# Kernel optimization log

Hardware: AMD Instinct MI355X
Metric: run time of the kernel (lower is better)

Reference implementation:

```python
import jax, jax.numpy as jnp
import numpy as np

EPS = 1e-5

def _ln(x, g, b):
    mu = jnp.mean(x, -1, keepdims=True)
    var = jnp.mean(jnp.square(x - mu), -1, keepdims=True)
    return (x - mu) * jax.lax.rsqrt(var + EPS) * g + b

def _switch_moe(h, gw, gb, W1, b1, W2, b2):
    # h: [B,T,D]; top-1 switch routing over E experts
    probs = jax.nn.softmax(h @ gw + gb, axis=-1)        # [B,T,E]
    idx = jnp.argmax(probs, axis=-1)                    # [B,T]
    p = jnp.max(probs, axis=-1)[..., None]              # [B,T,1] top-1 gate prob
    out = jnp.zeros_like(h)
    E = W1.shape[0]
    for e in range(E):  # small fixed expert count
        y = jax.nn.gelu(h @ W1[e] + b1[e]) @ W2[e] + b2[e]
        out = out + jnp.where((idx == e)[..., None], p * y, 0.0)
    return out

def setup_inputs() -> dict:
    key = jax.random.key(0)
    B, T, D, F, E, TE, NB = 64, 196, 512, 2048, 8, 512, 2
    ks = jax.random.split(key, 16)
    s = 0.02
    return {
        "x": jax.random.normal(ks[0], (B, T, D), jnp.float32),
        "emb": jax.random.normal(ks[1], (B, TE), jnp.float32),
        "ln_g": jnp.ones((NB, D), jnp.float32),
        "ln_b": jnp.zeros((NB, D), jnp.float32),
        "gate_w": jax.random.normal(ks[2], (NB, D, E), jnp.float32) * s,
        "gate_b": jnp.zeros((NB, E), jnp.float32),
        "w1": jax.random.normal(ks[3], (NB, E, D, F), jnp.float32) * s,
        "b1": jnp.zeros((NB, E, F), jnp.float32),
        "w2": jax.random.normal(ks[4], (NB, E, F, D), jnp.float32) * s,
        "b2": jnp.zeros((NB, E, D), jnp.float32),
        "emb_w": jax.random.normal(ks[5], (TE, 2 * D), jnp.float32) * s,
        "emb_b": jnp.zeros((2 * D,), jnp.float32),
        "sn_g": jnp.ones((D,), jnp.float32),
        "sn_b": jnp.zeros((D,), jnp.float32),
        "out_w": jax.random.normal(ks[6], (D, D), jnp.float32) * s,
        "out_b": jnp.zeros((D,), jnp.float32),
    }

def reference(x, emb, ln_g, ln_b, gate_w, gate_b, w1, b1, w2, b2,
              emb_w, emb_b, sn_g, sn_b, out_w, out_b):
    NB = ln_g.shape[0]
    out = jnp.zeros_like(x)
    for br in range(NB):  # fixed small branch count; dropout = identity (eval)
        h = _ln(x, ln_g[br], ln_b[br])
        out = out + _switch_moe(h, gate_w[br], gate_b[br], w1[br], b1[br], w2[br], b2[br])
    out = out / NB
    # StylizationBlock (FiLM): norm, scale/shift from time emb, SiLU+Linear, residual
    eo = jax.nn.silu(emb) @ emb_w + emb_b            # [B,2D]
    scale, shift = jnp.split(eo[:, None, :], 2, axis=-1)  # [B,1,D] each
    h = _ln(out, sn_g, sn_b) * (1.0 + scale) + shift
    h = jax.nn.silu(h) @ out_w + out_b
    return x + h
```

## Files before the change

### kernel.cpp

```cpp
#include <hip/hip_runtime.h>
#include <hip/hip_bf16.h>

typedef unsigned short u16;
typedef unsigned int u32;

typedef short bf16v8 __attribute__((ext_vector_type(8)));
typedef float f32v4 __attribute__((ext_vector_type(4)));

constexpr int BB   = 64;
constexpr int TT   = 196;
constexpr int NTOK = BB * TT;
constexpr int DD   = 512;
constexpr int FF   = 2048;
constexpr int EE   = 8;
constexpr int NBR  = 2;
constexpr int GE   = NBR * EE;
constexpr int MT128 = 212;

__device__ __forceinline__ u16 f2bf(float f) {
    union { float f; u32 u; } v; v.f = f;
    u32 r = v.u + 0x7fffu + ((v.u >> 16) & 1u);
    return (u16)(r >> 16);
}

__device__ __forceinline__ float bf2f(u32 u) {
    union { u32 u; float f; } v; v.u = u << 16; return v.f;
}

__device__ __forceinline__ float wave_sum(float v) {
    #pragma unroll
    for (int m = 32; m > 0; m >>= 1) v += __shfl_xor(v, m, 64);
    return v;
}

__device__ __forceinline__ float gelu_tanh(float v) {
    float y = 1.595769122f * v + 0.071354816f * (v * v * v);
    return v / (1.0f + __expf(-y));
}

__device__ __forceinline__ float silu(float v) {
    return v / (1.0f + __expf(-v));
}

__device__ __forceinline__ void gload16(const u16* g, u16* l) {
    typedef const __attribute__((address_space(1))) unsigned gv_t;
    typedef __attribute__((address_space(3))) unsigned lv_t;
    __builtin_amdgcn_global_load_lds((gv_t*)g, (lv_t*)l, 16, 0, 0);
}

__device__ __forceinline__ void bar() {
    asm volatile("" ::: "memory");
    __builtin_amdgcn_s_barrier();
    asm volatile("" ::: "memory");
}

#define ASM_VMCNT4 asm volatile("s_waitcnt vmcnt(4)" ::: "memory")
#define ASM_VMCNT0 asm volatile("s_waitcnt vmcnt(0)" ::: "memory")
#define ASM_LGKM0  asm volatile("s_waitcnt lgkmcnt(0)" ::: "memory")

__global__ __launch_bounds__(256) void mtrans_eo_kernel(
    const float* __restrict__ w1, u16* __restrict__ w1t,
    const float* __restrict__ w2, u16* __restrict__ w2t,
    const float* __restrict__ ow, u16* __restrict__ owt,
    const float* __restrict__ emb, const float* __restrict__ emb_w,
    const float* __restrict__ emb_b, float* __restrict__ eo,
    int* __restrict__ cnt)
{
    __shared__ float tile[64][69];
    __shared__ float se[4][DD];
    int id = blockIdx.x;
    int t = threadIdx.x;

    if (id >= 8256) {
        int id2 = id - 8256;
        int cg = id2 & 3, bg = id2 >> 2;
        int b0 = bg * 4;
        int c0 = cg * 256 + t;
        for (int i = t; i < 4 * DD; i += 256) {
            int b = i >> 9, d = i & (DD - 1);
            se[b][d] = silu(emb[(size_t)(b0 + b) * DD + d]);
        }
        __syncthreads();
        float acc[4] = {0, 0, 0, 0};
        for (int k = 0; k < DD; ++k) {
            float wv = emb_w[(size_t)k * 1024 + c0];
            #pragma unroll
            for (int b = 0; b < 4; ++b) acc[b] += se[b][k] * wv;
        }
        float bb = emb_b[c0];
        #pragma unroll
        for (int b = 0; b < 4; ++b)
            eo[(size_t)(b0 + b) * 1024 + c0] = acc[b] + bb;
        return;
    }

    if (id == 0 && t < 16) cnt[t] = 0;

    const float* src; u16* dst; int R, C, rt, ct;
    if (id < 4096) {
        int e = id >> 8, rem = id & 255;
        R = DD; C = FF; rt = rem >> 5; ct = rem & 31;
        src = w1 + (size_t)e * R * C; dst = w1t + (size_t)e * R * C;
    } else if (id < 8192) {
        int e = (id - 4096) >> 8, rem = (id - 4096) & 255;
        R = FF; C = DD; rt = rem >> 3; ct = rem & 7;
        src = w2 + (size_t)e * R * C; dst = w2t + (size_t)e * R * C;
    } else {
        int rem = id - 8192;
        R = DD; C = DD; rt = rem >> 3; ct = rem & 7;
        src = ow; dst = owt;
    }
    int tx = t & 15, ty = t >> 4;
    int r0 = rt * 64, c0 = ct * 64;
    #pragma unroll
    for (int j = 0; j < 4; ++j) {
        int row = ty + j * 16;
        float4 v = *(const float4*)&src[(size_t)(r0 + row) * C + c0 + tx * 4];
        tile[row][tx * 4 + 0] = v.x;
        tile[row][tx * 4 + 1] = v.y;
        tile[row][tx * 4 + 2] = v.z;
        tile[row][tx * 4 + 3] = v.w;
    }
    __syncthreads();
    int wc = t & 7, wr0 = t >> 3;
    #pragma unroll
    for (int p = 0; p < 2; ++p) {
        int cc = wr0 + p * 32;
        u16 pk[8];
        #pragma unroll
        for (int i = 0; i < 8; ++i)
            pk[i] = f2bf(tile[wc * 8 + i][cc]);
        uint4 v;
        v.x = (u32)pk[0] | ((u32)pk[1] << 16);
        v.y = (u32)pk[2] | ((u32)pk[3] << 16);
        v.z = (u32)pk[4] | ((u32)pk[5] << 16);
        v.w = (u32)pk[6] | ((u32)pk[7] << 16);
        *(uint4*)&dst[(size_t)(c0 + cc) * R + r0 + wc * 8] = v;
    }
}

__global__ __launch_bounds__(256) void ln_gate_kernel(
    const float* __restrict__ x, const float* __restrict__ ln_g, const float* __restrict__ ln_b,
    const float* __restrict__ gate_w, const float* __restrict__ gate_b,
    u16* __restrict__ hA, u16* __restrict__ hB,
    int* __restrict__ idxb, float* __restrict__ pbuf)
{
    int wave = threadIdx.x >> 6, lane = threadIdx.x & 63;
    int tok = blockIdx.x * 4 + wave;
    const float* xr = x + (size_t)tok * DD + lane * 8;
    float4 v0 = *(const float4*)xr;
    float4 v1 = *(const float4*)(xr + 4);
    float xs[8] = {v0.x, v0.y, v0.z, v0.w, v1.x, v1.y, v1.z, v1.w};
    float s = 0.f, ss = 0.f;
    #pragma unroll
    for (int i = 0; i < 8; ++i) { s += xs[i]; ss += xs[i] * xs[i]; }
    s = wave_sum(s); ss = wave_sum(ss);
    float mu = s * (1.0f / DD);
    float var = ss * (1.0f / DD) - mu * mu;
    float rstd = rsqrtf(var + 1e-5f);

    #pragma unroll
    for (int br = 0; br < NBR; ++br) {
        u16* hb = br ? hB : hA;
        float part[8] = {0, 0, 0, 0, 0, 0, 0, 0};
        u16 hu[8];
        #pragma unroll
        for (int i = 0; i < 8; ++i) {
            int d = lane * 8 + i;
            float g = ln_g[br * DD + d], b = ln_b[br * DD + d];
            float h = (xs[i] - mu) * rstd * g + b;
            hu[i] = f2bf(h);
            const float* gw = gate_w + ((size_t)br * DD + d) * EE;
            float4 g0 = *(const float4*)gw;
            float4 g1 = *(const float4*)(gw + 4);
            part[0] += h * g0.x; part[1] += h * g0.y; part[2] += h * g0.z; part[3] += h * g0.w;
            part[4] += h * g1.x; part[5] += h * g1.y; part[6] += h * g1.z; part[7] += h * g1.w;
        }
        uint4 pk;
        pk.x = (u32)hu[0] | ((u32)hu[1] << 16);
        pk.y = (u32)hu[2] | ((u32)hu[3] << 16);
        pk.z = (u32)hu[4] | ((u32)hu[5] << 16);
        pk.w = (u32)hu[6] | ((u32)hu[7] << 16);
        *(uint4*)(hb + (size_t)tok * DD + lane * 8) = pk;

        float logit[8];
        #pragma unroll
        for (int e = 0; e < 8; ++e)
            logit[e] = wave_sum(part[e]) + gate_b[br * EE + e];
        float m = logit[0]; int bi = 0;
        #pragma unroll
        for (int e = 1; e < 8; ++e)
            if (logit[e] > m) { m = logit[e]; bi = e; }
        float sum = 0.f;
        #pragma unroll
        for (int e = 0; e < 8; ++e) sum += __expf(logit[e] - m);
        if (lane == 0) {
            idxb[br * NTOK + tok] = bi;
            pbuf[br * NTOK + tok] = 1.0f / sum;
        }
    }
}

__global__ __launch_bounds__(256) void route_kernel(
    const int* __restrict__ idxb, int* __restrict__ cnt, int* __restrict__ list)
{
    __shared__ int lcnt[GE];
    __shared__ int gbase[GE];
    int tid = threadIdx.x;
    int t = blockIdx.x * 256 + tid;
    if (tid < GE) lcnt[tid] = 0;
    __syncthreads();
    int e0 = idxb[t];
    int e1 = EE + idxb[NTOK + t];
    int r0 = atomicAdd(&lcnt[e0], 1);
    int r1 = atomicAdd(&lcnt[e1], 1);
    __syncthreads();
    if (tid < GE) {
        int c = lcnt[tid];
        gbase[tid] = c ? atomicAdd(&cnt[tid], c) : 0;
    }
    __syncthreads();
    list[(size_t)e0 * NTOK + gbase[e0] + r0] = t;
    list[(size_t)e1 * NTOK + gbase[e1] + r1] = t;
}

__global__ void tilestart_kernel(const int* __restrict__ cnt, int* __restrict__ meta)
{
    int lane = threadIdx.x;
    if (lane < 16) {
        int pbv = 0;
        for (int k = 0; k < lane; ++k) pbv += cnt[k];
        meta[lane] = pbv;
    }
    if (lane == 16) {
        int n = 0;
        for (int k = 0; k < 16; ++k) n += (cnt[k] + 127) >> 7;
        meta[33] = n;
    }
    for (int j = lane; j < MT128; j += 64) {
        int ge = -1, start = 0, tt = 0;
        #pragma unroll
        for (int k = 0; k < 16; ++k) {
            int mt = (cnt[k] + 127) >> 7;
            if (ge < 0) {
                if (j < start + mt) { ge = k; tt = j - start; }
                else start += mt;
            }
        }
        if (ge >= 0) meta[64 + j] = (ge << 20) | tt;
    }
}

template<int MODE>
__global__ __launch_bounds__(256, 3) void gemm_tile(
    const u16* __restrict__ A0, const u16* __restrict__ A1,
    const u16* __restrict__ Bt,
    const int* __restrict__ meta, const int* __restrict__ cnt,
    const int* __restrict__ list, const float* __restrict__ pbuf,
    const float* __restrict__ bias,
    u16* __restrict__ uout, u16* __restrict__ moeout,
    const float* __restrict__ xres, float* __restrict__ dout)
{
    constexpr int K = (MODE == 1) ? FF : DD;
    constexpr int N = (MODE == 0) ? FF : DD;
    constexpr int NSTEP = K / 32;

    __shared__ __align__(16) u16 As[2][128 * 32];
    __shared__ __align__(16) u16 Bs[2][128 * 32];
    __shared__ int rowtok[128];
    __shared__ float rowp[128];

    int ntile = blockIdx.x;
    int ge = 0, rb = 0, cnt_e = 1 << 30, pb = 0;
    if constexpr (MODE != 2) {
        int j = blockIdx.y;
        if (j >= meta[33]) return;
        int ev = meta[64 + j];
        ge = ev >> 20;
        rb = (ev & 0xfffff) << 7;
        cnt_e = cnt[ge];
        pb = meta[ge];
    } else {
        rb = blockIdx.y * 128;
    }

    int tid = threadIdx.x, wave = tid >> 6, lane = tid & 63;
    int wm = wave >> 1, wn = wave & 1;
    int fr = lane & 15, fq = lane >> 4;
    int r0 = wave * 16 + (lane >> 2);
    int sc = (lane & 3) ^ ((lane >> 3) & 3);

    const u16* Abase;
    if constexpr (MODE == 0) Abase = (ge >= 8) ? A1 : A0;
    else                     Abase = A0;
    const u16* Bte = Bt + ((MODE == 2) ? (size_t)0 : (size_t)ge * FF * DD);

    const u16 *aSrc0, *aSrc1, *bSrc0, *bSrc1;
    if constexpr (MODE == 0) {
        int lb = ge * NTOK;
        int g0 = rb + r0, g1 = g0 + 64;
        int t0 = (g0 < cnt_e) ? list[lb + g0] : list[lb];
        int t1 = (g1 < cnt_e) ? list[lb + g1] : list[lb];
        aSrc0 = Abase + (size_t)t0 * K + sc * 8;
        aSrc1 = Abase + (size_t)t1 * K + sc * 8;
    } else {
        size_t base = (MODE == 1) ? (size_t)(pb + rb) : (size_t)rb;
        aSrc0 = Abase + (base + r0) * (size_t)K + sc * 8;
        aSrc1 = Abase + (base + r0 + 64) * (size_t)K + sc * 8;
    }
    {
        int nrow = ntile * 128 + r0;
        bSrc0 = Bte + (size_t)nrow * K + sc * 8;
        bSrc1 = Bte + (size_t)(nrow + 64) * K + sc * 8;
    }

    if constexpr (MODE == 1) {
        if (tid < 128) {
            int g = rb + tid;
            int tk = (g < cnt_e) ? list[ge * NTOK + g] : -1;
            rowtok[tid] = tk;
            rowp[tid] = (tk >= 0) ? pbuf[(ge >> 3) * NTOK + tk] : 0.f;
        }
        ASM_LGKM0;
    }

    f32v4 acc[4][4];
    #pragma unroll
    for (int mi = 0; mi < 4; ++mi)
        #pragma unroll
        for (int ni = 0; ni < 4; ++ni)
            acc[mi][ni] = (f32v4){0.f, 0.f, 0.f, 0.f};

    int ch = fq ^ ((fr >> 1) & 3);

    gload16(aSrc0, &As[0][wave * 512]);
    gload16(aSrc1, &As[0][2048 + wave * 512]);
    gload16(bSrc0, &Bs[0][wave * 512]);
    gload16(bSrc1, &Bs[0][2048 + wave * 512]);
    aSrc0 += 32; aSrc1 += 32; bSrc0 += 32; bSrc1 += 32;

    #pragma unroll 2
    for (int t = 0; t < NSTEP; ++t) {
        const int cur = t & 1;
        if (t + 1 < NSTEP) {
            gload16(aSrc0, &As[cur ^ 1][wave * 512]);
            gload16(aSrc1, &As[cur ^ 1][2048 + wave * 512]);
            gload16(bSrc0, &Bs[cur ^ 1][wave * 512]);
            gload16(bSrc1, &Bs[cur ^ 1][2048 + wave * 512]);
            aSrc0 += 32; aSrc1 += 32; bSrc0 += 32; bSrc1 += 32;
            ASM_VMCNT4;
        } else {
            ASM_VMCNT0;
        }
        bar();

        bf16v8 af[4], bfr[4];
        #pragma unroll
        for (int mi = 0; mi < 4; ++mi)
            af[mi] = *(const bf16v8*)&As[cur][(wm * 64 + mi * 16 + fr) * 32 + ch * 8];
        #pragma unroll
        for (int ni = 0; ni < 4; ++ni)
            bfr[ni] = *(const bf16v8*)&Bs[cur][(wn * 64 + ni * 16 + fr) * 32 + ch * 8];
        #pragma unroll
        for (int mi = 0; mi < 4; ++mi)
            #pragma unroll
            for (int ni = 0; ni < 4; ++ni)
                acc[mi][ni] = __builtin_amdgcn_mfma_f32_16x16x32_bf16(
                    af[mi], bfr[ni], acc[mi][ni], 0, 0, 0);
        bar();
    }

    #pragma unroll
    for (int mi = 0; mi < 4; ++mi) {
        #pragma unroll
        for (int ni = 0; ni < 4; ++ni) {
            int col = ntile * 128 + wn * 64 + ni * 16 + fr;
            float bn = (MODE == 2) ? bias[col] : bias[(size_t)ge * N + col];
            #pragma unroll
            for (int r = 0; r < 4; ++r) {
                int rr = wm * 64 + mi * 16 + fq * 4 + r;
                float v = acc[mi][ni][r] + bn;
                if constexpr (MODE == 0) {
                    if (rb + rr < cnt_e)
                        uout[(size_t)(pb + rb + rr) * FF + col] = f2bf(gelu_tanh(v));
                } else if constexpr (MODE == 1) {
                    int tok = rowtok[rr];
                    if (tok >= 0)
                        moeout[((size_t)(ge >> 3) * NTOK + tok) * DD + col] =
                            f2bf(v * rowp[rr]);
                } else {
                    size_t o = (size_t)(rb + rr) * DD + col;
                    dout[o] = xres[o] + v;
                }
            }
        }
    }
}

__global__ __launch_bounds__(256) void stylize_kernel(
    const u16* __restrict__ moe, const float* __restrict__ eo,
    const float* __restrict__ sn_g, const float* __restrict__ sn_b,
    u16* __restrict__ sbuf)
{
    int wave = threadIdx.x >> 6, lane = threadIdx.x & 63;
    int tok = blockIdx.x * 4 + wave;
    int b = tok / TT;
    const u16* mr = moe + (size_t)tok * DD + lane * 8;
    const u16* mr2 = mr + (size_t)NTOK * DD;
    uint4 pa = *(const uint4*)mr;
    uint4 pb = *(const uint4*)mr2;
    float os[8];
    os[0] = (bf2f(pa.x & 0xffff) + bf2f(pb.x & 0xffff)) * 0.5f;
    os[1] = (bf2f(pa.x >> 16)    + bf2f(pb.x >> 16))    * 0.5f;
    os[2] = (bf2f(pa.y & 0xffff) + bf2f(pb.y & 0xffff)) * 0.5f;
    os[3] = (bf2f(pa.y >> 16)    + bf2f(pb.y >> 16))    * 0.5f;
    os[4] = (bf2f(pa.z & 0xffff) + bf2f(pb.z & 0xffff)) * 0.5f;
    os[5] = (bf2f(pa.z >> 16)    + bf2f(pb.z >> 16))    * 0.5f;
    os[6] = (bf2f(pa.w & 0xffff) + bf2f(pb.w & 0xffff)) * 0.5f;
    os[7] = (bf2f(pa.w >> 16)    + bf2f(pb.w >> 16))    * 0.5f;
    float s = 0.f, ss = 0.f;
    #pragma unroll
    for (int i = 0; i < 8; ++i) { s += os[i]; ss += os[i] * os[i]; }
    s = wave_sum(s); ss = wave_sum(ss);
    float mu = s * (1.0f / DD);
    float var = ss * (1.0f / DD) - mu * mu;
    float rstd = rsqrtf(var + 1e-5f);
    u16 hu[8];
    #pragma unroll
    for (int i = 0; i < 8; ++i) {
        int d = lane * 8 + i;
        float h = (os[i] - mu) * rstd * sn_g[d] + sn_b[d];
        float scv = eo[(size_t)b * 1024 + d];
        float shv = eo[(size_t)b * 1024 + DD + d];
        h = h * (1.0f + scv) + shv;
        hu[i] = f2bf(silu(h));
    }
    uint4 pk;
    pk.x = (u32)hu[0] | ((u32)hu[1] << 16);
    pk.y = (u32)hu[2] | ((u32)hu[3] << 16);
    pk.z = (u32)hu[4] | ((u32)hu[5] << 16);
    pk.w = (u32)hu[6] | ((u32)hu[7] << 16);
    *(uint4*)(sbuf + (size_t)tok * DD + lane * 8) = pk;
}

extern "C" void kernel_launch(void* const* d_in, const int* in_sizes, int n_in,
                              void* d_out, int out_size, void* d_ws, size_t ws_size,
                              hipStream_t stream)
{
    const float* x      = (const float*)d_in[0];
    const float* emb    = (const float*)d_in[1];
    const float* ln_g   = (const float*)d_in[2];
    const float* ln_b   = (const float*)d_in[3];
    const float* gate_w = (const float*)d_in[4];
    const float* gate_b = (const float*)d_in[5];
    const float* w1     = (const float*)d_in[6];
    const float* b1     = (const float*)d_in[7];
    const float* w2     = (const float*)d_in[8];
    const float* b2     = (const float*)d_in[9];
    const float* emb_w  = (const float*)d_in[10];
    const float* emb_b  = (const float*)d_in[11];
    const float* sn_g   = (const float*)d_in[12];
    const float* sn_b   = (const float*)d_in[13];
    const float* out_w  = (const float*)d_in[14];
    const float* out_b  = (const float*)d_in[15];
    (void)n_in; (void)in_sizes; (void)out_size; (void)ws_size;

    const size_t szW    = (size_t)GE * FF * DD * 2;
    const size_t szOwt  = (size_t)DD * DD * 2;
    const size_t szH    = (size_t)NTOK * DD * 2;
    const size_t szEo   = (size_t)BB * 2 * DD * 4;
    const size_t szP    = (size_t)NBR * NTOK * 4;
    const size_t szCnt  = 256, szMeta = 4096;
    const size_t szList = (size_t)GE * NTOK * 4;
    const size_t szU    = ((size_t)2 * NTOK + 256) * FF * 2;
    const size_t szM    = (size_t)2 * NTOK * DD * 2;

    auto align256 = [](size_t v) { return (v + 255) & ~(size_t)255; };
    char* w = (char*)d_ws;
    size_t off = 0;
    auto take = [&](size_t bytes) -> void* {
        void* p = w + off;
        off = align256(off + bytes);
        return p;
    };
    u16*   w1t  = (u16*)take(szW);
    u16*   w2t  = (u16*)take(szW);
    u16*   owt  = (u16*)take(szOwt);
    u16*   hA   = (u16*)take(szH);
    u16*   hB   = (u16*)take(szH);
    float* eo   = (float*)take(szEo);
    float* pbuf = (float*)take(szP);
    int*   idxb = (int*)take(szP);
    int*   cnt  = (int*)take(szCnt);
    int*   meta = (int*)take(szMeta);
    int*   list = (int*)take(szList);
    u16*   ubuf = (u16*)take(szU);
    u16*   moe  = (u16*)take(szM);

    mtrans_eo_kernel<<<8320, 256, 0, stream>>>(w1, w1t, w2, w2t, out_w, owt,
                                               emb, emb_w, emb_b, eo, cnt);

    ln_gate_kernel<<<NTOK / 4, 256, 0, stream>>>(x, ln_g, ln_b, gate_w, gate_b,
                                                 hA, hB, idxb, pbuf);

    route_kernel<<<NTOK / 256, 256, 0, stream>>>(idxb, cnt, list);
    tilestart_kernel<<<1, 64, 0, stream>>>(cnt, meta);

    gemm_tile<0><<<dim3(FF / 128, MT128), 256, 0, stream>>>(
        hA, hB, w1t, meta, cnt, list, nullptr, b1, ubuf, nullptr, nullptr, nullptr);
    gemm_tile<1><<<dim3(DD / 128, MT128), 256, 0, stream>>>(
        ubuf, nullptr, w2t, meta, cnt, list, pbuf, b2, nullptr, moe, nullptr, nullptr);

    stylize_kernel<<<NTOK / 4, 256, 0, stream>>>(moe, eo, sn_g, sn_b, hA);
    gemm_tile<2><<<dim3(DD / 128, NTOK / 128), 256, 0, stream>>>(
        hA, nullptr, owt, nullptr, nullptr, nullptr, nullptr, out_b,
        nullptr, nullptr, x, (float*)d_out);
}
```

Before: 370.9 us.

## Enlarge expert GEMM tiles to 256x256 with 512-thread blocks

The two routed expert GEMMs move from 128x128 tiles (256 threads) to 256x256 tiles (512 threads, 8 waves, each computing 128x64). Tile-start metadata is recomputed at 256-row granularity and the ubuf padding is enlarged to match. The output projection GEMM is split into its own specialised kernel. The larger tiles aim to raise operand reuse and cut global and LDS traffic per flop. The cost is fewer blocks (the second GEMM gets only about two hundred), more padded rows per expert, and heavy accumulator register pressure that may spill or limit occupancy.

```diff
diff --git a/kernel.cpp b/kernel.cpp
--- a/kernel.cpp
+++ b/kernel.cpp
@@ -15,7 +15,7 @@
 constexpr int EE   = 8;
 constexpr int NBR  = 2;
 constexpr int GE   = NBR * EE;
-constexpr int MT128 = 212;
+constexpr int MT256 = 114;
 
 __device__ __forceinline__ u16 f2bf(float f) {
     union { float f; u32 u; } v; v.f = f;
@@ -232,57 +232,169 @@
         for (int k = 0; k < lane; ++k) pbv += cnt[k];
         meta[lane] = pbv;
     }
-    if (lane == 16) {
+    if (lane == 17) {
         int n = 0;
-        for (int k = 0; k < 16; ++k) n += (cnt[k] + 127) >> 7;
-        meta[33] = n;
-    }
-    for (int j = lane; j < MT128; j += 64) {
+        for (int k = 0; k < 16; ++k) n += (cnt[k] + 255) >> 8;
+        meta[34] = n;
+    }
+    for (int j = lane; j < MT256; j += 64) {
         int ge = -1, start = 0, tt = 0;
         #pragma unroll
         for (int k = 0; k < 16; ++k) {
-            int mt = (cnt[k] + 127) >> 7;
+            int mt = (cnt[k] + 255) >> 8;
             if (ge < 0) {
                 if (j < start + mt) { ge = k; tt = j - start; }
                 else start += mt;
             }
         }
-        if (ge >= 0) meta[64 + j] = (ge << 20) | tt;
+        if (ge >= 0) meta[320 + j] = (ge << 20) | tt;
     }
 }
 
 template<int MODE>
-__global__ __launch_bounds__(256, 3) void gemm_tile(
+__global__ __launch_bounds__(512, 2) void gemm256(
     const u16* __restrict__ A0, const u16* __restrict__ A1,
     const u16* __restrict__ Bt,
     const int* __restrict__ meta, const int* __restrict__ cnt,
     const int* __restrict__ list, const float* __restrict__ pbuf,
     const float* __restrict__ bias,
-    u16* __restrict__ uout, u16* __restrict__ moeout,
-    const float* __restrict__ xres, float* __restrict__ dout)
+    u16* __restrict__ uout, u16* __restrict__ moeout)
 {
     constexpr int K = (MODE == 1) ? FF : DD;
     constexpr int N = (MODE == 0) ? FF : DD;
     constexpr int NSTEP = K / 32;
 
+    __shared__ __align__(16) u16 As[2][256 * 32];
+    __shared__ __align__(16) u16 Bs[2][256 * 32];
+    __shared__ int rowtok[256];
+    __shared__ float rowp[256];
+
+    int j = blockIdx.y;
+    if (j >= meta[34]) return;
+    int ev = meta[320 + j];
+    int ge = ev >> 20;
+    int rb = (ev & 0xfffff) << 8;
+    int cnt_e = cnt[ge];
+    int pb = meta[ge];
+    int ntile = blockIdx.x;
+
+    int tid = threadIdx.x, wave = tid >> 6, lane = tid & 63;
+    int wm = wave >> 2, wn = wave & 3;
+    int fr = lane & 15, fq = lane >> 4;
+    int sc = (lane & 3) ^ ((lane >> 3) & 3);
+
+    const u16* Bte = Bt + (size_t)ge * FF * DD;
+
+    int ar0 = wave * 32 + (lane >> 2);
+    const u16 *aS0, *aS1, *bS0, *bS1;
+    if constexpr (MODE == 0) {
+        const u16* Ab = (ge >= 8) ? A1 : A0;
+        int lb = ge * NTOK;
+        int g0 = rb + ar0, g1 = g0 + 16;
+        int t0 = (g0 < cnt_e) ? list[lb + g0] : list[lb];
+        int t1 = (g1 < cnt_e) ? list[lb + g1] : list[lb];
+        aS0 = Ab + (size_t)t0 * K + sc * 8;
+        aS1 = Ab + (size_t)t1 * K + sc * 8;
+    } else {
+        aS0 = A0 + (size_t)(pb + rb + ar0) * K + sc * 8;
+        aS1 = aS0 + (size_t)16 * K;
+    }
+    {
+        int nr = ntile * 256 + ar0;
+        bS0 = Bte + (size_t)nr * K + sc * 8;
+        bS1 = bS0 + (size_t)16 * K;
+    }
+
+    if constexpr (MODE == 1) {
+        if (tid < 256) {
+            int g = rb + tid;
+            int tk = (g < cnt_e) ? list[ge * NTOK + g] : -1;
+            rowtok[tid] = tk;
+            rowp[tid] = (tk >= 0) ? pbuf[(ge >> 3) * NTOK + tk] : 0.f;
+        }
+    }
+
+    f32v4 acc[8][4];
+    #pragma unroll
+    for (int m = 0; m < 8; ++m)
+        #pragma unroll
+        for (int n = 0; n < 4; ++n)
+            acc[m][n] = (f32v4){0.f, 0.f, 0.f, 0.f};
+
+    int ch = fq ^ ((fr >> 1) & 3);
+    int dA = wave * 1024;
+
+    gload16(aS0, &As[0][dA]);
+    gload16(aS1, &As[0][dA + 512]);
+    gload16(bS0, &Bs[0][dA]);
+    gload16(bS1, &Bs[0][dA + 512]);
+    aS0 += 32; aS1 += 32; bS0 += 32; bS1 += 32;
+
+    for (int t = 0; t < NSTEP; ++t) {
+        const int cur = t & 1;
+        if (t + 1 < NSTEP) {
+            gload16(aS0, &As[cur ^ 1][dA]);
+            gload16(aS1, &As[cur ^ 1][dA + 512]);
+            gload16(bS0, &Bs[cur ^ 1][dA]);
+            gload16(bS1, &Bs[cur ^ 1][dA + 512]);
+            aS0 += 32; aS1 += 32; bS0 += 32; bS1 += 32;
+            ASM_VMCNT4;
+        } else {
+            ASM_VMCNT0;
+        }
+        bar();
+
+        bf16v8 bf[4];
+        #pragma unroll
+        for (int n = 0; n < 4; ++n)
+            bf[n] = *(const bf16v8*)&Bs[cur][(wn * 64 + n * 16 + fr) * 32 + ch * 8];
+        #pragma unroll
+        for (int m = 0; m < 8; ++m) {
+            bf16v8 af = *(const bf16v8*)&As[cur][(wm * 128 + m * 16 + fr) * 32 + ch * 8];
+            #pragma unroll
+            for (int n = 0; n < 4; ++n)
+                acc[m][n] = __builtin_amdgcn_mfma_f32_16x16x32_bf16(af, bf[n], acc[m][n], 0, 0, 0);
+        }
+        bar();
+    }
+
+    #pragma unroll
+    for (int m = 0; m < 8; ++m) {
+        #pragma unroll
+        for (int n = 0; n < 4; ++n) {
+            int col = ntile * 256 + wn * 64 + n * 16 + fr;
+            float bn = bias[(size_t)ge * N + col];
+            #pragma unroll
+            for (int r = 0; r < 4; ++r) {
+                int rr = wm * 128 + m * 16 + fq * 4 + r;
+                float v = acc[m][n][r] + bn;
+                if constexpr (MODE == 0) {
+                    if (rb + rr < cnt_e)
+                        uout[(size_t)(pb + rb + rr) * FF + col] = f2bf(gelu_tanh(v));
+                } else {
+                    int tok = rowtok[rr];
+                    if (tok >= 0)
+                        moeout[((size_t)(ge >> 3) * NTOK + tok) * DD + col] =
+                            f2bf(v * rowp[rr]);
+                }
+            }
+        }
+    }
+}
+
+__global__ __launch_bounds__(256, 3) void gemm_out(
+    const u16* __restrict__ A0, const u16* __restrict__ Bt,
+    const float* __restrict__ bias,
+    const float* __restrict__ xres, float* __restrict__ dout)
+{
+    constexpr int K = DD;
+    constexpr int NSTEP = K / 32;
+
     __shared__ __align__(16) u16 As[2][128 * 32];
     __shared__ __align__(16) u16 Bs[2][128 * 32];
-    __shared__ int rowtok[128];
-    __shared__ float rowp[128];
 
     int ntile = blockIdx.x;
-    int ge = 0, rb = 0, cnt_e = 1 << 30, pb = 0;
-    if constexpr (MODE != 2) {
-        int j = blockIdx.y;
-        if (j >= meta[33]) return;
-        int ev = meta[64 + j];
-        ge = ev >> 20;
-        rb = (ev & 0xfffff) << 7;
-        cnt_e = cnt[ge];
-        pb = meta[ge];
-    } else {
-        rb = blockIdx.y * 128;
-    }
+    int rb = blockIdx.y * 128;
 
     int tid = threadIdx.x, wave = tid >> 6, lane = tid & 63;
     int wm = wave >> 1, wn = wave & 1;
@@ -290,38 +402,13 @@
     int r0 = wave * 16 + (lane >> 2);
     int sc = (lane & 3) ^ ((lane >> 3) & 3);
 
-    const u16* Abase;
-    if constexpr (MODE == 0) Abase = (ge >= 8) ? A1 : A0;
-    else                     Abase = A0;
-    const u16* Bte = Bt + ((MODE == 2) ? (size_t)0 : (size_t)ge * FF * DD);
-
     const u16 *aSrc0, *aSrc1, *bSrc0, *bSrc1;
-    if constexpr (MODE == 0) {
-        int lb = ge * NTOK;
-        int g0 = rb + r0, g1 = g0 + 64;
-        int t0 = (g0 < cnt_e) ? list[lb + g0] : list[lb];
-        int t1 = (g1 < cnt_e) ? list[lb + g1] : list[lb];
-        aSrc0 = Abase + (size_t)t0 * K + sc * 8;
-        aSrc1 = Abase + (size_t)t1 * K + sc * 8;
-    } else {
-        size_t base = (MODE == 1) ? (size_t)(pb + rb) : (size_t)rb;
-        aSrc0 = Abase + (base + r0) * (size_t)K + sc * 8;
-        aSrc1 = Abase + (base + r0 + 64) * (size_t)K + sc * 8;
-    }
+    aSrc0 = A0 + (size_t)(rb + r0) * K + sc * 8;
+    aSrc1 = A0 + (size_t)(rb + r0 + 64) * K + sc * 8;
     {
         int nrow = ntile * 128 + r0;
-        bSrc0 = Bte + (size_t)nrow * K + sc * 8;
-        bSrc1 = Bte + (size_t)(nrow + 64) * K + sc * 8;
-    }
-
-    if constexpr (MODE == 1) {
-        if (tid < 128) {
-            int g = rb + tid;
-            int tk = (g < cnt_e) ? list[ge * NTOK + g] : -1;
-            rowtok[tid] = tk;
-            rowp[tid] = (tk >= 0) ? pbuf[(ge >> 3) * NTOK + tk] : 0.f;
-        }
-        ASM_LGKM0;
+        bSrc0 = Bt + (size_t)nrow * K + sc * 8;
+        bSrc1 = Bt + (size_t)(nrow + 64) * K + sc * 8;
     }
 
     f32v4 acc[4][4];
@@ -375,23 +462,12 @@
         #pragma unroll
         for (int ni = 0; ni < 4; ++ni) {
             int col = ntile * 128 + wn * 64 + ni * 16 + fr;
-            float bn = (MODE == 2) ? bias[col] : bias[(size_t)ge * N + col];
+            float bn = bias[col];
             #pragma unroll
             for (int r = 0; r < 4; ++r) {
                 int rr = wm * 64 + mi * 16 + fq * 4 + r;
-                float v = acc[mi][ni][r] + bn;
-                if constexpr (MODE == 0) {
-                    if (rb + rr < cnt_e)
-                        uout[(size_t)(pb + rb + rr) * FF + col] = f2bf(gelu_tanh(v));
-                } else if constexpr (MODE == 1) {
-                    int tok = rowtok[rr];
-                    if (tok >= 0)
-                        moeout[((size_t)(ge >> 3) * NTOK + tok) * DD + col] =
-                            f2bf(v * rowp[rr]);
-                } else {
-                    size_t o = (size_t)(rb + rr) * DD + col;
-                    dout[o] = xres[o] + v;
-                }
+                size_t o = (size_t)(rb + rr) * DD + col;
+                dout[o] = xres[o] + acc[mi][ni][r] + bn;
             }
         }
     }
@@ -472,7 +548,7 @@
     const size_t szP    = (size_t)NBR * NTOK * 4;
     const size_t szCnt  = 256, szMeta = 4096;
     const size_t szList = (size_t)GE * NTOK * 4;
-    const size_t szU    = ((size_t)2 * NTOK + 256) * FF * 2;
+    const size_t szU    = ((size_t)2 * NTOK + 512) * FF * 2;
     const size_t szM    = (size_t)2 * NTOK * DD * 2;
 
     auto align256 = [](size_t v) { return (v + 255) & ~(size_t)255; };
@@ -506,13 +582,12 @@
     route_kernel<<<NTOK / 256, 256, 0, stream>>>(idxb, cnt, list);
     tilestart_kernel<<<1, 64, 0, stream>>>(cnt, meta);
 
-    gemm_tile<0><<<dim3(FF / 128, MT128), 256, 0, stream>>>(
-        hA, hB, w1t, meta, cnt, list, nullptr, b1, ubuf, nullptr, nullptr, nullptr);
-    gemm_tile<1><<<dim3(DD / 128, MT128), 256, 0, stream>>>(
-        ubuf, nullptr, w2t, meta, cnt, list, pbuf, b2, nullptr, moe, nullptr, nullptr);
+    gemm256<0><<<dim3(FF / 256, MT256), 512, 0, stream>>>(
+        hA, hB, w1t, meta, cnt, list, nullptr, b1, ubuf, nullptr);
+    gemm256<1><<<dim3(DD / 256, MT256), 512, 0, stream>>>(
+        ubuf, nullptr, w2t, meta, cnt, list, pbuf, b2, nullptr, moe);
 
     stylize_kernel<<<NTOK / 4, 256, 0, stream>>>(moe, eo, sn_g, sn_b, hA);
-    gemm_tile<2><<<dim3(DD / 128, NTOK / 128), 256, 0, stream>>>(
-        hA, nullptr, owt, nullptr, nullptr, nullptr, nullptr, out_b,
-        nullptr, nullptr, x, (float*)d_out);
-}
+    gemm_out<<<dim3(DD / 128, NTOK / 128), 256, 0, stream>>>(
+        hA, owt, out_b, x, (float*)d_out);
+}
```

Result: slower. 397.4 us (+7.2%).
